# Kernel tuning notes

Hardware: AMD Instinct MI355X
Metric: run time of the kernel (lower is better)

## Reference

```python
import jax, jax.numpy as jnp
import numpy as np

GN_GROUPS = 32
GN_EPS = 1e-5
K = 3  # deform kernel size, padding=1, dilation=1


def conv1x1(x, w):  # x [B,C,H,W], w [O,C]
    return jnp.einsum('bchw,oc->bohw', x, w)


def conv3x3(x, w):  # w [O,I,3,3], stride 1, pad 1
    return jax.lax.conv_general_dilated(
        x, w, window_strides=(1, 1), padding=((1, 1), (1, 1)),
        dimension_numbers=('NCHW', 'OIHW', 'NCHW'))


def group_norm(x, gamma, beta):
    B, C, H, W = x.shape
    xg = x.reshape(B, GN_GROUPS, C // GN_GROUPS, H, W)
    mu = xg.mean(axis=(2, 3, 4), keepdims=True)
    var = xg.var(axis=(2, 3, 4), keepdims=True)
    xn = ((xg - mu) * jax.lax.rsqrt(var + GN_EPS)).reshape(B, C, H, W)
    return xn * gamma[None, :, None, None] + beta[None, :, None, None]


def deform_conv(x, offset, w):
    """DeformConv v1, kernel 3, pad 1, deformable_groups=1.
    x [B,C,H,W]; offset [B,18,H,W] as (dy,dx) per kernel tap; w [O,C,3,3]."""
    B, C, H, W = x.shape
    off = offset.reshape(B, K * K, 2, H, W)
    dy, dx = off[:, :, 0], off[:, :, 1]                      # [B,9,H,W]
    ky, kx = jnp.meshgrid(jnp.arange(K) - 1, jnp.arange(K) - 1, indexing='ij')
    ky = ky.reshape(1, K * K, 1, 1).astype(x.dtype)
    kx = kx.reshape(1, K * K, 1, 1).astype(x.dtype)
    gy = jnp.arange(H, dtype=x.dtype).reshape(1, 1, H, 1)
    gx = jnp.arange(W, dtype=x.dtype).reshape(1, 1, 1, W)
    py = gy + ky + dy                                        # [B,9,H,W] sample y
    px = gx + kx + dx                                        # [B,9,H,W] sample x

    y0 = jnp.floor(py); x0 = jnp.floor(px)
    wy1 = py - y0; wy0 = 1.0 - wy1
    wx1 = px - x0; wx0 = 1.0 - wx1
    xf = x.reshape(B, C, H * W)

    def corner(yc, xc, wgt):
        valid = (yc >= 0) & (yc < H) & (xc >= 0) & (xc < W)  # zero padding outside
        yi = jnp.clip(yc, 0, H - 1).astype(jnp.int32)
        xi = jnp.clip(xc, 0, W - 1).astype(jnp.int32)
        idx = (yi * W + xi).reshape(B, -1)                   # [B, 9*H*W]
        v = jax.vmap(lambda f, i: f[:, i])(xf, idx)          # [B, C, 9*H*W]
        v = v.reshape(B, C, K * K, H, W)
        return v * (wgt * valid.astype(x.dtype))[:, None]

    sampled = (corner(y0, x0, wy0 * wx0) + corner(y0, x0 + 1, wy0 * wx1)
               + corner(y0 + 1, x0, wy1 * wx0) + corner(y0 + 1, x0 + 1, wy1 * wx1))
    # contract sampled [B,C,9,H,W] with weights [O,C,9]
    return jnp.einsum('bckhw,ock->bohw', sampled, w.reshape(w.shape[0], C, K * K))


def setup_inputs() -> dict:
    key = jax.random.key(0)
    ks = jax.random.split(key, 8)
    B, Cc, H, W = 4, 256, 128, 128
    ci = Cc // 4  # 64
    x = jax.random.normal(ks[0], (B, Cc, H, W), dtype=jnp.float32)
    w1 = jax.random.normal(ks[1], (ci, Cc), dtype=jnp.float32) * 0.05
    g1 = jnp.ones((ci,), jnp.float32); b1 = jnp.zeros((ci,), jnp.float32)
    w_off = jax.random.normal(ks[2], (18, ci, 3, 3), dtype=jnp.float32) * 0.01
    w_def = jax.random.normal(ks[3], (ci, ci, 3, 3), dtype=jnp.float32) * 0.05
    w3 = jax.random.normal(ks[4], (Cc, ci), dtype=jnp.float32) * 0.05
    g3 = jnp.ones((Cc,), jnp.float32); b3 = jnp.zeros((Cc,), jnp.float32)
    return {'x': x, 'w1': w1, 'g1': g1, 'b1': b1, 'w_off': w_off,
            'w_def': w_def, 'w3': w3, 'g3': g3, 'b3': b3}


def reference(x, w1, g1, b1, w_off, w_def, w3, g3, b3):
    xd = jax.nn.relu(group_norm(conv1x1(x, w1), g1, b1))     # scale1
    offset1 = conv3x3(xd, w_off)                              # off_conva
    out1 = deform_conv(xd, offset1, w_def)                    # kernel_conva
    out = out1 + xd
    out = jax.nn.relu(group_norm(conv1x1(out, w3), g3, b3)) + x  # scale3 + residual
    return out
```

## Files before the change

kernel.cpp:

```cpp
#include <hip/hip_runtime.h>


#define HW 16384
#define WIDTH 128

typedef __attribute__((ext_vector_type(8))) short bf16x8;
typedef __attribute__((ext_vector_type(4))) float f32x4;

__device__ __forceinline__ unsigned short f2bf(float f) {
  unsigned int u = __float_as_uint(f);
  u = (u + 0x7fffu + ((u >> 16) & 1u)) >> 16;
  return (unsigned short)u;
}
__device__ __forceinline__ float bflo(unsigned int u) { return __uint_as_float(u << 16); }
__device__ __forceinline__ float bfhi(unsigned int u) { return __uint_as_float(u & 0xffff0000u); }

__global__ __launch_bounds__(256) void k_prep(const float* __restrict__ w1, const float* __restrict__ w3,
                                              const float* __restrict__ wdef, const float* __restrict__ woff,
                                              unsigned short* __restrict__ wA1f,
                                              unsigned short* __restrict__ wBf,
                                              unsigned short* __restrict__ wofBf,
                                              unsigned short* __restrict__ w3Bf) {
  int i = blockIdx.x * 256 + threadIdx.x;
  if (i < 16384) {
    int j = i & 7;
    int lane = (i >> 3) & 63;
    int m = (i >> 9) & 3;
    int kt = i >> 11;
    int o = (m << 4) + (lane & 15);
    int c = kt * 32 + ((lane >> 4) << 3) + j;
    wA1f[i] = f2bf(w1[(size_t)o * 256 + c]);
  }
  if (i < 36864) {
    int j = i & 7;
    int lane = (i >> 3) & 63;
    int n = (i >> 9) & 3;
    int kt = i >> 11;
    int kk = kt * 32 + ((lane >> 4) << 3) + j;
    int tap = kk >> 6, c = kk & 63;
    int o = (n << 4) + (lane & 15);
    wBf[i] = f2bf(wdef[(size_t)o * 576 + c * 9 + tap]);
  }
  if (i < 18432) {
    int j = i & 7;
    int lane = (i >> 3) & 63;
    int n = (i >> 9) & 1;
    int kt = i >> 10;
    int kk = kt * 32 + ((lane >> 4) << 3) + j;
    int tap = kk >> 6, c = kk & 63;
    int o = (n << 4) + (lane & 15);
    wofBf[i] = (o < 18) ? f2bf(woff[((size_t)(o * 64 + c)) * 9 + tap]) : (unsigned short)0;
  }
  if (i < 32768) {
    int j = i & 7;
    int lane = (i >> 3) & 63;
    int n = (i >> 9) & 15;
    int kt = i >> 13;
    int c = kt * 32 + ((lane >> 4) << 3) + j;
    int o = (n << 4) + (lane & 15);
    w3Bf[i] = f2bf(w3[(size_t)o * 64 + c]);
  }
}

__global__ __launch_bounds__(256) void k_conv1m(const float* __restrict__ x,
                                                const unsigned short* __restrict__ wA1f,
                                                unsigned short* __restrict__ xdT, float* __restrict__ ps) {
  __shared__ unsigned short xs[2][64][72];
  __shared__ float lds_s[4][32], lds_ss[4][32];
  int tid = threadIdx.x;
  int wave = tid >> 6, lane = tid & 63;
  int b = blockIdx.x >> 8;
  int chunk = blockIdx.x & 255;
  int px0 = chunk << 6;
  int pxl = lane & 15, q = lane >> 4;
  const float* xb = x + (size_t)b * 256 * HW + px0;
  const bf16x8* wAp = (const bf16x8*)wA1f;
  int sc = tid >> 4;
  int sq = tid & 15;
  f32x4 acc[4];
#pragma unroll
  for (int m = 0; m < 4; m++) acc[m] = (f32x4){0.f, 0.f, 0.f, 0.f};

  float4 vr[4];
#pragma unroll
  for (int r = 0; r < 4; r++)
    vr[r] = *(const float4*)(xb + (size_t)(r * 16 + sc) * HW + sq * 4);
#pragma unroll
  for (int r = 0; r < 4; r++) {
    int c = r * 16 + sc;
    xs[0][sq * 4 + 0][c] = f2bf(vr[r].x);
    xs[0][sq * 4 + 1][c] = f2bf(vr[r].y);
    xs[0][sq * 4 + 2][c] = f2bf(vr[r].z);
    xs[0][sq * 4 + 3][c] = f2bf(vr[r].w);
  }
  __syncthreads();

  for (int cb = 0; cb < 4; cb++) {
    int cur = cb & 1;
    if (cb < 3) {
#pragma unroll
      for (int r = 0; r < 4; r++)
        vr[r] = *(const float4*)(xb + (size_t)((cb + 1) * 64 + r * 16 + sc) * HW + sq * 4);
    }
#pragma unroll
    for (int kt = 0; kt < 2; kt++) {
      bf16x8 bfrag = *(const bf16x8*)&xs[cur][wave * 16 + pxl][kt * 32 + q * 8];
      int ktG = cb * 2 + kt;
#pragma unroll
      for (int m = 0; m < 4; m++) {
        bf16x8 af = wAp[(ktG * 4 + m) * 64 + lane];
        acc[m] = __builtin_amdgcn_mfma_f32_16x16x32_bf16(af, bfrag, acc[m], 0, 0, 0);
      }
    }
    if (cb < 3) {
#pragma unroll
      for (int r = 0; r < 4; r++) {
        int c = r * 16 + sc;
        xs[cur ^ 1][sq * 4 + 0][c] = f2bf(vr[r].x);
        xs[cur ^ 1][sq * 4 + 1][c] = f2bf(vr[r].y);
        xs[cur ^ 1][sq * 4 + 2][c] = f2bf(vr[r].z);
        xs[cur ^ 1][sq * 4 + 3][c] = f2bf(vr[r].w);
      }
    }
    __syncthreads();
  }
  unsigned short* xo = xdT + ((size_t)b * HW + px0 + wave * 16 + pxl) * 64 + (q << 2);
#pragma unroll
  for (int m = 0; m < 4; m++) {
    unsigned int u0, u1;
    asm("v_cvt_pk_bf16_f32 %0, %1, %2" : "=v"(u0) : "v"(acc[m][0]), "v"(acc[m][1]));
    asm("v_cvt_pk_bf16_f32 %0, %1, %2" : "=v"(u1) : "v"(acc[m][2]), "v"(acc[m][3]));
    *(uint2*)(xo + m * 16) = make_uint2(u0, u1);
  }
  float s[8], sq2[8];
#pragma unroll
  for (int m = 0; m < 4; m++)
#pragma unroll
    for (int h = 0; h < 2; h++) {
      float a = acc[m][2 * h] + acc[m][2 * h + 1];
      float qq = acc[m][2 * h] * acc[m][2 * h] + acc[m][2 * h + 1] * acc[m][2 * h + 1];
      s[m * 2 + h] = a; sq2[m * 2 + h] = qq;
    }
#pragma unroll
  for (int i = 0; i < 8; i++) {
#pragma unroll
    for (int off = 8; off; off >>= 1) {
      s[i] += __shfl_down(s[i], off, 16);
      sq2[i] += __shfl_down(sq2[i], off, 16);
    }
  }
  if (pxl == 0) {
#pragma unroll
    for (int i = 0; i < 8; i++) {
      int m = i >> 1, h = i & 1;
      int g = m * 8 + q * 2 + h;
      lds_s[wave][g] = s[i];
      lds_ss[wave][g] = sq2[i];
    }
  }
  __syncthreads();
  if (tid < 32) {
    float S = lds_s[0][tid] + lds_s[1][tid] + lds_s[2][tid] + lds_s[3][tid];
    float SS = lds_ss[0][tid] + lds_ss[1][tid] + lds_ss[2][tid] + lds_ss[3][tid];
    int bg = b * 32 + tid;
    ps[(bg * 256 + chunk) * 2] = S;
    ps[(bg * 256 + chunk) * 2 + 1] = SS;
  }
}

__global__ __launch_bounds__(256) void k_gnfin_p(const float* __restrict__ ps, float* __restrict__ mrs,
                                                 int S, float n) {
  int bg = blockIdx.x;
  float s = 0.f, ss = 0.f;
  for (int i = threadIdx.x; i < S; i += 256) { s += ps[(bg * S + i) * 2]; ss += ps[(bg * S + i) * 2 + 1]; }
#pragma unroll
  for (int off = 32; off; off >>= 1) { s += __shfl_down(s, off); ss += __shfl_down(ss, off); }
  __shared__ float ls[4], lss[4];
  int wv = threadIdx.x >> 6;
  if ((threadIdx.x & 63) == 0) { ls[wv] = s; lss[wv] = ss; }
  __syncthreads();
  if (threadIdx.x == 0) {
    float Sa = ls[0] + ls[1] + ls[2] + ls[3];
    float SSa = lss[0] + lss[1] + lss[2] + lss[3];
    float mu = Sa / n;
    float var = SSa / n - mu * mu;
    mrs[bg] = mu;
    mrs[128 + bg] = rsqrtf(var + 1e-5f);
  }
}

__global__ __launch_bounds__(256) void k_gnapply_bf(unsigned short* __restrict__ xdT,
                                                    const float* __restrict__ mrs,
                                                    const float* __restrict__ g1, const float* __restrict__ b1) {
  int i = blockIdx.x * 256 + threadIdx.x;
  int b = i >> 17;
  int ck = i & 7;
  int c0 = ck << 3;
  uint4 v = ((const uint4*)xdT)[i];
  float ga[8], be[8];
#pragma unroll
  for (int j = 0; j < 8; j += 2) {
    int g = (c0 + j) >> 1;
    float mu = mrs[b * 32 + g], rs = mrs[128 + b * 32 + g];
    ga[j] = g1[c0 + j] * rs;     be[j] = b1[c0 + j] - mu * ga[j];
    ga[j + 1] = g1[c0 + j + 1] * rs; be[j + 1] = b1[c0 + j + 1] - mu * ga[j + 1];
  }
  float r[8];
  r[0] = fmaxf(bflo(v.x) * ga[0] + be[0], 0.f);
  r[1] = fmaxf(bfhi(v.x) * ga[1] + be[1], 0.f);
  r[2] = fmaxf(bflo(v.y) * ga[2] + be[2], 0.f);
  r[3] = fmaxf(bfhi(v.y) * ga[3] + be[3], 0.f);
  r[4] = fmaxf(bflo(v.z) * ga[4] + be[4], 0.f);
  r[5] = fmaxf(bfhi(v.z) * ga[5] + be[5], 0.f);
  r[6] = fmaxf(bflo(v.w) * ga[6] + be[6], 0.f);
  r[7] = fmaxf(bfhi(v.w) * ga[7] + be[7], 0.f);
  uint4 o;
  asm("v_cvt_pk_bf16_f32 %0, %1, %2" : "=v"(o.x) : "v"(r[0]), "v"(r[1]));
  asm("v_cvt_pk_bf16_f32 %0, %1, %2" : "=v"(o.y) : "v"(r[2]), "v"(r[3]));
  asm("v_cvt_pk_bf16_f32 %0, %1, %2" : "=v"(o.z) : "v"(r[4]), "v"(r[5]));
  asm("v_cvt_pk_bf16_f32 %0, %1, %2" : "=v"(o.w) : "v"(r[6]), "v"(r[7]));
  ((uint4*)xdT)[i] = o;
}

__global__ __launch_bounds__(576, 7) void k_mega(const unsigned short* __restrict__ xdT,
                                                 const unsigned short* __restrict__ wofBf,
                                                 const unsigned short* __restrict__ wBf,
                                                 const unsigned short* __restrict__ w3Bf,
                                                 unsigned short* __restrict__ t3,
                                                 float* __restrict__ ps2) {
  __shared__ unsigned short A[36 * 65 * 8];
  __shared__ float offsL[64 * 18];
  int tid = threadIdx.x;
  int bb = blockIdx.x >> 8;
  int tileid = blockIdx.x & 255;
  int px0 = tileid << 6;
  const unsigned short* xtf = xdT + (size_t)bb * 64 * HW;
  const char* xbt = (const char*)xtf;
  int wave = tid >> 6;
  int lane = tid & 63;
  int q16 = lane >> 2;
  int ch4 = lane & 3;
  int kcbyte = (wave * 4 + ch4) * 1040;
  int kq = lane >> 4;

  f32x4 aoff = {0.f, 0.f, 0.f, 0.f};
  {
    int ky = wave / 3 - 1, kx = wave % 3 - 1;
    int n2 = wave & 1;
    int mh1 = wave >> 1;
    int r1 = mh1 * 16 + (lane & 15);
    for (int h = 0; h < 2; ++h) {
      int co = (h << 6) + (ch4 << 4);
#pragma unroll
      for (int g = 0; g < 4; ++g) {
        int src = (g << 4) + q16;
        int px = px0 + src;
        int sy = (px >> 7) + ky;
        int sx = (px & 127) + kx;
        bool valid = ((unsigned)sy < 128u) && ((unsigned)sx < 128u);
        uint4 v = make_uint4(0u, 0u, 0u, 0u);
        if (valid) v = *(const uint4*)(xbt + (((sy << 7) + sx) << 7) + co);
        *(uint4*)((char*)A + kcbyte + src * 16) = v;
      }
      __syncthreads();
      if (wave < 8) {
        const bf16x8* wp = (const bf16x8*)wofBf;
        __builtin_amdgcn_s_setprio(1);
#pragma unroll
        for (int tap = 0; tap < 9; ++tap) {
          bf16x8 bk = wp[((2 * tap + h) * 2 + n2) * 64 + lane];
          bf16x8 a0 = *(const bf16x8*)((const char*)A + ((tap * 4 + kq) * 65 + r1) * 16);
          aoff = __builtin_amdgcn_mfma_f32_16x16x32_bf16(a0, bk, aoff, 0, 0, 0);
        }
        __builtin_amdgcn_s_setprio(0);
      }
      __syncthreads();
    }
    if (wave < 8) {
      int o = n2 * 16 + (lane & 15);
      if (o < 18) {
        int prow = mh1 * 16 + ((lane >> 4) << 2);
#pragma unroll
        for (int r = 0; r < 4; r++) offsL[(prow + r) * 18 + o] = aoff[r];
      }
    }
  }
  __syncthreads();

  float w00, w01, w10, w11;
  int a00, a01, a10, a11;
  {
    int px = px0 + lane;
    int y = px >> 7, xc = px & 127;
    float dy = offsL[lane * 18 + 2 * wave];
    float dx = offsL[lane * 18 + 2 * wave + 1];
    float py = (float)(y + wave / 3 - 1) + dy;
    float pxx = (float)(xc + wave % 3 - 1) + dx;
    float y0f = floorf(py), x0f = floorf(pxx);
    float ay = py - y0f, ax = pxx - x0f;
    int y0 = (int)y0f, x0 = (int)x0f;
    int y1i = y0 + 1, x1i = x0 + 1;
    float by0 = 1.f - ay, bx0 = 1.f - ax;
    bool vy0 = (unsigned)y0 < 128u, vy1 = (unsigned)y1i < 128u;
    bool vx0 = (unsigned)x0 < 128u, vx1 = (unsigned)x1i < 128u;
    w00 = (vy0 && vx0) ? by0 * bx0 : 0.f;
    w01 = (vy0 && vx1) ? by0 * ax : 0.f;
    w10 = (vy1 && vx0) ? ay * bx0 : 0.f;
    w11 = (vy1 && vx1) ? ay * ax : 0.f;
    int iy0 = min(max(y0, 0), 127), iy1 = min(max(y1i, 0), 127);
    int ix0 = min(max(x0, 0), 127), ix1 = min(max(x1i, 0), 127);
    a00 = (iy0 * WIDTH + ix0) << 7;
    a01 = (iy0 * WIDTH + ix1) << 7;
    a10 = (iy1 * WIDTH + ix0) << 7;
    a11 = (iy1 * WIDTH + ix1) << 7;
  }

  int n1 = wave & 3;
  int mh = wave >> 2;
  f32x4 acc0 = {0.f, 0.f, 0.f, 0.f};
  f32x4 acc1 = {0.f, 0.f, 0.f, 0.f};
  for (int h = 0; h < 2; ++h) {
    int co = (h << 6) + (ch4 << 4);
#pragma unroll
    for (int g = 0; g < 4; ++g) {
      int src = (g << 4) + q16;
      float j0 = __shfl(w00, src), j1 = __shfl(w01, src);
      float j2 = __shfl(w10, src), j3 = __shfl(w11, src);
      int b0 = __shfl(a00, src), b1 = __shfl(a01, src);
      int b2 = __shfl(a10, src), b3 = __shfl(a11, src);
      uint4 v0 = *(const uint4*)(xbt + b0 + co);
      uint4 v1 = *(const uint4*)(xbt + b1 + co);
      uint4 v2 = *(const uint4*)(xbt + b2 + co);
      uint4 v3 = *(const uint4*)(xbt + b3 + co);
      float r[8];
      r[0] = j0 * bflo(v0.x) + j1 * bflo(v1.x) + j2 * bflo(v2.x) + j3 * bflo(v3.x);
      r[1] = j0 * bfhi(v0.x) + j1 * bfhi(v1.x) + j2 * bfhi(v2.x) + j3 * bfhi(v3.x);
      r[2] = j0 * bflo(v0.y) + j1 * bflo(v1.y) + j2 * bflo(v2.y) + j3 * bflo(v3.y);
      r[3] = j0 * bfhi(v0.y) + j1 * bfhi(v1.y) + j2 * bfhi(v2.y) + j3 * bfhi(v3.y);
      r[4] = j0 * bflo(v0.z) + j1 * bflo(v1.z) + j2 * bflo(v2.z) + j3 * bflo(v3.z);
      r[5] = j0 * bfhi(v0.z) + j1 * bfhi(v1.z) + j2 * bfhi(v2.z) + j3 * bfhi(v3.z);
      r[6] = j0 * bflo(v0.w) + j1 * bflo(v1.w) + j2 * bflo(v2.w) + j3 * bflo(v3.w);
      r[7] = j0 * bfhi(v0.w) + j1 * bfhi(v1.w) + j2 * bfhi(v2.w) + j3 * bfhi(v3.w);
      uint4 ov;
      asm("v_cvt_pk_bf16_f32 %0, %1, %2" : "=v"(ov.x) : "v"(r[0]), "v"(r[1]));
      asm("v_cvt_pk_bf16_f32 %0, %1, %2" : "=v"(ov.y) : "v"(r[2]), "v"(r[3]));
      asm("v_cvt_pk_bf16_f32 %0, %1, %2" : "=v"(ov.z) : "v"(r[4]), "v"(r[5]));
      asm("v_cvt_pk_bf16_f32 %0, %1, %2" : "=v"(ov.w) : "v"(r[6]), "v"(r[7]));
      *(uint4*)((char*)A + kcbyte + src * 16) = ov;
    }
    __syncthreads();
    if (wave < 8) {
      int r0r = mh * 32 + (lane & 15);
      const bf16x8* wp = (const bf16x8*)wBf;
      __builtin_amdgcn_s_setprio(1);
#pragma unroll
      for (int tap = 0; tap < 9; ++tap) {
        bf16x8 bk = wp[((2 * tap + h) * 4 + n1) * 64 + lane];
        int kc = tap * 4 + kq;
        bf16x8 a0 = *(const bf16x8*)((const char*)A + (kc * 65 + r0r) * 16);
        bf16x8 a1 = *(const bf16x8*)((const char*)A + (kc * 65 + r0r + 16) * 16);
        acc0 = __builtin_amdgcn_mfma_f32_16x16x32_bf16(a0, bk, acc0, 0, 0, 0);
        acc1 = __builtin_amdgcn_mfma_f32_16x16x32_bf16(a1, bk, acc1, 0, 0, 0);
      }
      __builtin_amdgcn_s_setprio(0);
    }
    __syncthreads();
  }
  if (wave < 8) {
    int c = n1 * 16 + (lane & 15);
    int pb = px0 + mh * 32 + ((lane >> 4) << 2);
#pragma unroll
    for (int r = 0; r < 4; r++) {
      acc0[r] += __uint_as_float((unsigned int)xtf[(size_t)(pb + r) * 64 + c] << 16);
      acc1[r] += __uint_as_float((unsigned int)xtf[(size_t)(pb + 16 + r) * 64 + c] << 16);
    }
    char* base = (char*)A + (c >> 3) * 1040 + (c & 7) * 2;
    int pxr = mh * 32 + ((lane >> 4) << 2);
#pragma unroll
    for (int r = 0; r < 4; r++) {
      *(unsigned short*)(base + (size_t)(pxr + r) * 16) = f2bf(acc0[r]);
      *(unsigned short*)(base + (size_t)(pxr + 16 + r) * 16) = f2bf(acc1[r]);
    }
  }
  __syncthreads();
  if (wave >= 8) return;

  f32x4 cA[4], cB[4];
#pragma unroll
  for (int ni = 0; ni < 4; ni++) {
    cA[ni] = (f32x4){0.f, 0.f, 0.f, 0.f};
    cB[ni] = (f32x4){0.f, 0.f, 0.f, 0.f};
  }
  {
    int mt0 = (wave >> 2) * 2;
    const bf16x8* wp2 = (const bf16x8*)w3Bf;
    __builtin_amdgcn_s_setprio(1);
#pragma unroll
    for (int kt = 0; kt < 2; kt++) {
      int kc = kt * 4 + kq;
      bf16x8 aA = *(const bf16x8*)((const char*)A + (size_t)(kc * 65 + mt0 * 16 + (lane & 15)) * 16);
      bf16x8 aB = *(const bf16x8*)((const char*)A + (size_t)(kc * 65 + (mt0 + 1) * 16 + (lane & 15)) * 16);
#pragma unroll
      for (int ni = 0; ni < 4; ni++) {
        int ng = n1 * 4 + ni;
        bf16x8 bk = wp2[(kt * 16 + ng) * 64 + lane];
        cA[ni] = __builtin_amdgcn_mfma_f32_16x16x32_bf16(aA, bk, cA[ni], 0, 0, 0);
        cB[ni] = __builtin_amdgcn_mfma_f32_16x16x32_bf16(aB, bk, cB[ni], 0, 0, 0);
      }
    }
    __builtin_amdgcn_s_setprio(0);
  }
#pragma unroll
  for (int ni = 0; ni < 4; ni++) {
    float s = 0.f, qq = 0.f;
#pragma unroll
    for (int r = 0; r < 4; r++) {
      float v0 = cA[ni][r], v1 = cB[ni][r];
      s += v0 + v1; qq += v0 * v0 + v1 * v1;
    }
    s += __shfl_down(s, 32); qq += __shfl_down(qq, 32);
    s += __shfl_down(s, 16); qq += __shfl_down(qq, 16);
    s += __shfl_down(s, 4);  qq += __shfl_down(qq, 4);
    s += __shfl_down(s, 2);  qq += __shfl_down(qq, 2);
    s += __shfl_down(s, 1);  qq += __shfl_down(qq, 1);
    if (lane == 0 || lane == 8) {
      int g = (n1 * 4 + ni) * 2 + (lane >> 3);
      int slot = ((bb * 32 + g) * 256 + tileid) * 2 + (wave >> 2);
      ps2[slot * 2] = s;
      ps2[slot * 2 + 1] = qq;
    }
  }
  unsigned short* tb = t3 + (size_t)bb * 256 * HW + px0;
  int mtq = (wave >> 2) * 32 + ((lane >> 4) << 2);
#pragma unroll
  for (int ni = 0; ni < 4; ni++) {
    int o = (n1 * 4 + ni) * 16 + (lane & 15);
    unsigned short* p0 = tb + (size_t)o * HW + mtq;
    unsigned int u0, u1, u2, u3;
    asm("v_cvt_pk_bf16_f32 %0, %1, %2" : "=v"(u0) : "v"(cA[ni][0]), "v"(cA[ni][1]));
    asm("v_cvt_pk_bf16_f32 %0, %1, %2" : "=v"(u1) : "v"(cA[ni][2]), "v"(cA[ni][3]));
    asm("v_cvt_pk_bf16_f32 %0, %1, %2" : "=v"(u2) : "v"(cB[ni][0]), "v"(cB[ni][1]));
    asm("v_cvt_pk_bf16_f32 %0, %1, %2" : "=v"(u3) : "v"(cB[ni][2]), "v"(cB[ni][3]));
    *(uint2*)p0 = make_uint2(u0, u1);
    *(uint2*)(p0 + 16) = make_uint2(u2, u3);
  }
}

__global__ __launch_bounds__(256) void k_final(const unsigned short* __restrict__ t3, const float* __restrict__ x,
                                               const float* __restrict__ mrs, const float* __restrict__ g3,
                                               const float* __restrict__ b3, float* __restrict__ out) {
  int i4 = blockIdx.x * 256 + threadIdx.x;
  int b = i4 >> 20;
  int c = (i4 >> 12) & 255;
  int g = c >> 3;
  float mu = mrs[b * 32 + g], rs = mrs[128 + b * 32 + g];
  float ga = g3[c] * rs, be = b3[c] - mu * ga;
  uint2 tv = ((const uint2*)t3)[i4];
  float t0 = bflo(tv.x);
  float t1 = bfhi(tv.x);
  float t2 = bflo(tv.y);
  float t3v = bfhi(tv.y);
  float4 xv = ((const float4*)x)[i4];
  float4 r;
  r.x = fmaxf(t0 * ga + be, 0.f) + xv.x;
  r.y = fmaxf(t1 * ga + be, 0.f) + xv.y;
  r.z = fmaxf(t2 * ga + be, 0.f) + xv.z;
  r.w = fmaxf(t3v * ga + be, 0.f) + xv.w;
  ((float4*)out)[i4] = r;
}

extern "C" void kernel_launch(void* const* d_in, const int* in_sizes, int n_in,
                              void* d_out, int out_size, void* d_ws, size_t ws_size,
                              hipStream_t stream) {
  const float* x    = (const float*)d_in[0];
  const float* w1   = (const float*)d_in[1];
  const float* g1   = (const float*)d_in[2];
  const float* b1   = (const float*)d_in[3];
  const float* woff = (const float*)d_in[4];
  const float* wdef = (const float*)d_in[5];
  const float* w3   = (const float*)d_in[6];
  const float* g3   = (const float*)d_in[7];
  const float* b3   = (const float*)d_in[8];
  float* ws = (float*)d_ws;

  unsigned short* xdT = (unsigned short*)ws;
  unsigned short* t3  = (unsigned short*)(ws + 2097152);
  float* base = ws + 2097152 + 8388608;
  float* mrs1 = base;
  float* mrs2 = mrs1 + 256;
  unsigned short* wA1f  = (unsigned short*)(mrs2 + 256);
  unsigned short* wBf   = (unsigned short*)(mrs2 + 256 + 8192);
  unsigned short* wofBf = (unsigned short*)(mrs2 + 256 + 8192 + 18432);
  unsigned short* w3Bf  = (unsigned short*)(mrs2 + 256 + 8192 + 18432 + 9216);
  float* ps   = mrs2 + 256 + 8192 + 18432 + 9216 + 16384;
  float* ps2  = ps + 65536;
  float* out  = (float*)d_out;

  hipLaunchKernelGGL(k_prep, dim3(144), dim3(256), 0, stream, w1, w3, wdef, woff, wA1f, wBf, wofBf, w3Bf);
  hipLaunchKernelGGL(k_conv1m, dim3(1024), dim3(256), 0, stream, x, wA1f, xdT, ps);
  hipLaunchKernelGGL(k_gnfin_p, dim3(128), dim3(256), 0, stream, ps, mrs1, 256, (float)(2 * HW));
  hipLaunchKernelGGL(k_gnapply_bf, dim3(2048), dim3(256), 0, stream, xdT, mrs1, g1, b1);
  hipLaunchKernelGGL(k_mega, dim3(1024), dim3(576), 0, stream, xdT, wofBf, wBf, w3Bf, t3, ps2);
  hipLaunchKernelGGL(k_gnfin_p, dim3(128), dim3(256), 0, stream, ps2, mrs2, 512, 131072.f);
  hipLaunchKernelGGL(k_final, dim3(16384), dim3(256), 0, stream, t3, x, mrs2, g3, b3, out);
}
```

Before: 111.1 us.

## Build deform-conv MFMA A operands in registers instead of staging through LDS

The bilinear sampling step is restructured so each wave computes sample coordinates and weights per tap for its own pixel row and packs the interpolated bf16 values directly into the MFMA A-fragment. This removes the shuffle-based distribution, the LDS write of the sampled matrix, and the two __syncthreads per half, and only waves 0-7 take part. The cost is that the waves sharing a row block each recompute the same sampling and gathers, and all 16 waves no longer share the gather work. Register pressure may also rise.

```diff
diff --git a/kernel.cpp b/kernel.cpp
--- a/kernel.cpp
+++ b/kernel.cpp
@@ -287,104 +287,91 @@
   }
   __syncthreads();
 
-  float w00, w01, w10, w11;
-  int a00, a01, a10, a11;
-  {
-    int px = px0 + lane;
-    int y = px >> 7, xc = px & 127;
-    float dy = offsL[lane * 18 + 2 * wave];
-    float dx = offsL[lane * 18 + 2 * wave + 1];
-    float py = (float)(y + wave / 3 - 1) + dy;
-    float pxx = (float)(xc + wave % 3 - 1) + dx;
-    float y0f = floorf(py), x0f = floorf(pxx);
-    float ay = py - y0f, ax = pxx - x0f;
-    int y0 = (int)y0f, x0 = (int)x0f;
-    int y1i = y0 + 1, x1i = x0 + 1;
-    float by0 = 1.f - ay, bx0 = 1.f - ax;
-    bool vy0 = (unsigned)y0 < 128u, vy1 = (unsigned)y1i < 128u;
-    bool vx0 = (unsigned)x0 < 128u, vx1 = (unsigned)x1i < 128u;
-    w00 = (vy0 && vx0) ? by0 * bx0 : 0.f;
-    w01 = (vy0 && vx1) ? by0 * ax : 0.f;
-    w10 = (vy1 && vx0) ? ay * bx0 : 0.f;
-    w11 = (vy1 && vx1) ? ay * ax : 0.f;
-    int iy0 = min(max(y0, 0), 127), iy1 = min(max(y1i, 0), 127);
-    int ix0 = min(max(x0, 0), 127), ix1 = min(max(x1i, 0), 127);
-    a00 = (iy0 * WIDTH + ix0) << 7;
-    a01 = (iy0 * WIDTH + ix1) << 7;
-    a10 = (iy1 * WIDTH + ix0) << 7;
-    a11 = (iy1 * WIDTH + ix1) << 7;
-  }
-
-  int n1 = wave & 3;
-  int mh = wave >> 2;
-  f32x4 acc0 = {0.f, 0.f, 0.f, 0.f};
-  f32x4 acc1 = {0.f, 0.f, 0.f, 0.f};
-  for (int h = 0; h < 2; ++h) {
-    int co = (h << 6) + (ch4 << 4);
-#pragma unroll
-    for (int g = 0; g < 4; ++g) {
-      int src = (g << 4) + q16;
-      float j0 = __shfl(w00, src), j1 = __shfl(w01, src);
-      float j2 = __shfl(w10, src), j3 = __shfl(w11, src);
-      int b0 = __shfl(a00, src), b1 = __shfl(a01, src);
-      int b2 = __shfl(a10, src), b3 = __shfl(a11, src);
-      uint4 v0 = *(const uint4*)(xbt + b0 + co);
-      uint4 v1 = *(const uint4*)(xbt + b1 + co);
-      uint4 v2 = *(const uint4*)(xbt + b2 + co);
-      uint4 v3 = *(const uint4*)(xbt + b3 + co);
-      float r[8];
-      r[0] = j0 * bflo(v0.x) + j1 * bflo(v1.x) + j2 * bflo(v2.x) + j3 * bflo(v3.x);
-      r[1] = j0 * bfhi(v0.x) + j1 * bfhi(v1.x) + j2 * bfhi(v2.x) + j3 * bfhi(v3.x);
-      r[2] = j0 * bflo(v0.y) + j1 * bflo(v1.y) + j2 * bflo(v2.y) + j3 * bflo(v3.y);
-      r[3] = j0 * bfhi(v0.y) + j1 * bfhi(v1.y) + j2 * bfhi(v2.y) + j3 * bfhi(v3.y);
-      r[4] = j0 * bflo(v0.z) + j1 * bflo(v1.z) + j2 * bflo(v2.z) + j3 * bflo(v3.z);
-      r[5] = j0 * bfhi(v0.z) + j1 * bfhi(v1.z) + j2 * bfhi(v2.z) + j3 * bfhi(v3.z);
-      r[6] = j0 * bflo(v0.w) + j1 * bflo(v1.w) + j2 * bflo(v2.w) + j3 * bflo(v3.w);
-      r[7] = j0 * bfhi(v0.w) + j1 * bfhi(v1.w) + j2 * bfhi(v2.w) + j3 * bfhi(v3.w);
-      uint4 ov;
-      asm("v_cvt_pk_bf16_f32 %0, %1, %2" : "=v"(ov.x) : "v"(r[0]), "v"(r[1]));
-      asm("v_cvt_pk_bf16_f32 %0, %1, %2" : "=v"(ov.y) : "v"(r[2]), "v"(r[3]));
-      asm("v_cvt_pk_bf16_f32 %0, %1, %2" : "=v"(ov.z) : "v"(r[4]), "v"(r[5]));
-      asm("v_cvt_pk_bf16_f32 %0, %1, %2" : "=v"(ov.w) : "v"(r[6]), "v"(r[7]));
-      *(uint4*)((char*)A + kcbyte + src * 16) = ov;
-    }
-    __syncthreads();
-    if (wave < 8) {
-      int r0r = mh * 32 + (lane & 15);
-      const bf16x8* wp = (const bf16x8*)wBf;
-      __builtin_amdgcn_s_setprio(1);
-#pragma unroll
-      for (int tap = 0; tap < 9; ++tap) {
-        bf16x8 bk = wp[((2 * tap + h) * 4 + n1) * 64 + lane];
-        int kc = tap * 4 + kq;
-        bf16x8 a0 = *(const bf16x8*)((const char*)A + (kc * 65 + r0r) * 16);
-        bf16x8 a1 = *(const bf16x8*)((const char*)A + (kc * 65 + r0r + 16) * 16);
-        acc0 = __builtin_amdgcn_mfma_f32_16x16x32_bf16(a0, bk, acc0, 0, 0, 0);
-        acc1 = __builtin_amdgcn_mfma_f32_16x16x32_bf16(a1, bk, acc1, 0, 0, 0);
-      }
-      __builtin_amdgcn_s_setprio(0);
-    }
-    __syncthreads();
-  }
+  f32x4 accA = {0.f, 0.f, 0.f, 0.f};
+  f32x4 accB = {0.f, 0.f, 0.f, 0.f};
+  int pxl = lane & 15;
+  int dmh = wave >> 1, dnh = wave & 1;
   if (wave < 8) {
-    int c = n1 * 16 + (lane & 15);
-    int pb = px0 + mh * 32 + ((lane >> 4) << 2);
+    int rowl = dmh * 16 + pxl;
+    int pxg = px0 + rowl;
+    int yy = pxg >> 7, xx = pxg & 127;
+    const bf16x8* wp = (const bf16x8*)wBf;
+#pragma unroll 2
+    for (int tap = 0; tap < 9; ++tap) {
+      float dy = offsL[rowl * 18 + 2 * tap];
+      float dx = offsL[rowl * 18 + 2 * tap + 1];
+      float py = (float)(yy + tap / 3 - 1) + dy;
+      float pxx = (float)(xx + tap % 3 - 1) + dx;
+      float y0f = floorf(py), x0f = floorf(pxx);
+      float ay = py - y0f, ax = pxx - x0f;
+      int y0 = (int)y0f, x0 = (int)x0f;
+      int y1i = y0 + 1, x1i = x0 + 1;
+      float by0 = 1.f - ay, bx0 = 1.f - ax;
+      bool vy0 = (unsigned)y0 < 128u, vy1 = (unsigned)y1i < 128u;
+      bool vx0 = (unsigned)x0 < 128u, vx1 = (unsigned)x1i < 128u;
+      float w00 = (vy0 && vx0) ? by0 * bx0 : 0.f;
+      float w01 = (vy0 && vx1) ? by0 * ax : 0.f;
+      float w10 = (vy1 && vx0) ? ay * bx0 : 0.f;
+      float w11 = (vy1 && vx1) ? ay * ax : 0.f;
+      int iy0 = min(max(y0, 0), 127), iy1 = min(max(y1i, 0), 127);
+      int ix0 = min(max(x0, 0), 127), ix1 = min(max(x1i, 0), 127);
+      int a00 = (iy0 * WIDTH + ix0) << 7;
+      int a01 = (iy0 * WIDTH + ix1) << 7;
+      int a10 = (iy1 * WIDTH + ix0) << 7;
+      int a11 = (iy1 * WIDTH + ix1) << 7;
+#pragma unroll
+      for (int h = 0; h < 2; ++h) {
+        int co = (h << 6) + (kq << 4);
+        uint4 v0 = *(const uint4*)(xbt + a00 + co);
+        uint4 v1 = *(const uint4*)(xbt + a01 + co);
+        uint4 v2 = *(const uint4*)(xbt + a10 + co);
+        uint4 v3 = *(const uint4*)(xbt + a11 + co);
+        float r[8];
+        r[0] = w00 * bflo(v0.x) + w01 * bflo(v1.x) + w10 * bflo(v2.x) + w11 * bflo(v3.x);
+        r[1] = w00 * bfhi(v0.x) + w01 * bfhi(v1.x) + w10 * bfhi(v2.x) + w11 * bfhi(v3.x);
+        r[2] = w00 * bflo(v0.y) + w01 * bflo(v1.y) + w10 * bflo(v2.y) + w11 * bflo(v3.y);
+        r[3] = w00 * bfhi(v0.y) + w01 * bfhi(v1.y) + w10 * bfhi(v2.y) + w11 * bfhi(v3.y);
+        r[4] = w00 * bflo(v0.z) + w01 * bflo(v1.z) + w10 * bflo(v2.z) + w11 * bflo(v3.z);
+        r[5] = w00 * bfhi(v0.z) + w01 * bfhi(v1.z) + w10 * bfhi(v2.z) + w11 * bfhi(v3.z);
+        r[6] = w00 * bflo(v0.w) + w01 * bflo(v1.w) + w10 * bflo(v2.w) + w11 * bflo(v3.w);
+        r[7] = w00 * bfhi(v0.w) + w01 * bfhi(v1.w) + w10 * bfhi(v2.w) + w11 * bfhi(v3.w);
+        bf16x8 af;
+        unsigned int u0, u1, u2, u3;
+        asm("v_cvt_pk_bf16_f32 %0, %1, %2" : "=v"(u0) : "v"(r[0]), "v"(r[1]));
+        asm("v_cvt_pk_bf16_f32 %0, %1, %2" : "=v"(u1) : "v"(r[2]), "v"(r[3]));
+        asm("v_cvt_pk_bf16_f32 %0, %1, %2" : "=v"(u2) : "v"(r[4]), "v"(r[5]));
+        asm("v_cvt_pk_bf16_f32 %0, %1, %2" : "=v"(u3) : "v"(r[6]), "v"(r[7]));
+        ((unsigned int*)&af)[0] = u0;
+        ((unsigned int*)&af)[1] = u1;
+        ((unsigned int*)&af)[2] = u2;
+        ((unsigned int*)&af)[3] = u3;
+        int kt = tap * 2 + h;
+        bf16x8 bk0 = wp[(kt * 4 + dnh * 2 + 0) * 64 + lane];
+        bf16x8 bk1 = wp[(kt * 4 + dnh * 2 + 1) * 64 + lane];
+        accA = __builtin_amdgcn_mfma_f32_16x16x32_bf16(af, bk0, accA, 0, 0, 0);
+        accB = __builtin_amdgcn_mfma_f32_16x16x32_bf16(af, bk1, accB, 0, 0, 0);
+      }
+    }
+    int c0 = dnh * 32 + pxl;
+    int pb = px0 + dmh * 16 + (kq << 2);
 #pragma unroll
     for (int r = 0; r < 4; r++) {
-      acc0[r] += __uint_as_float((unsigned int)xtf[(size_t)(pb + r) * 64 + c] << 16);
-      acc1[r] += __uint_as_float((unsigned int)xtf[(size_t)(pb + 16 + r) * 64 + c] << 16);
-    }
-    char* base = (char*)A + (c >> 3) * 1040 + (c & 7) * 2;
-    int pxr = mh * 32 + ((lane >> 4) << 2);
+      accA[r] += __uint_as_float((unsigned int)xtf[(size_t)(pb + r) * 64 + c0] << 16);
+      accB[r] += __uint_as_float((unsigned int)xtf[(size_t)(pb + r) * 64 + c0 + 16] << 16);
+    }
+    int pxr = dmh * 16 + (kq << 2);
+    char* bA = (char*)A + (c0 >> 3) * 1040 + (c0 & 7) * 2;
+    char* bB = (char*)A + ((c0 + 16) >> 3) * 1040 + ((c0 + 16) & 7) * 2;
 #pragma unroll
     for (int r = 0; r < 4; r++) {
-      *(unsigned short*)(base + (size_t)(pxr + r) * 16) = f2bf(acc0[r]);
-      *(unsigned short*)(base + (size_t)(pxr + 16 + r) * 16) = f2bf(acc1[r]);
+      *(unsigned short*)(bA + (size_t)(pxr + r) * 16) = f2bf(accA[r]);
+      *(unsigned short*)(bB + (size_t)(pxr + r) * 16) = f2bf(accB[r]);
     }
   }
   __syncthreads();
   if (wave >= 8) return;
 
+  int n1 = wave & 3;
   f32x4 cA[4], cB[4];
 #pragma unroll
   for (int ni = 0; ni < 4; ni++) {
```

Measured after the change: 154.0 us. +38.7%, slower.

## Drop ninth wave in deform mega kernel and alias offset buffer onto LDS tile

Applied to the files above, without the earlier changes.

Block size for the fused deform kernel goes from 576 to 512 threads. The ninth tap's gather and bilinear-sample work, previously done by its own wave, is spread across waves 0-3 as extra per-lane work. The separate shared offset buffer is removed and aliased onto the A tile, with an added barrier before A is overwritten. The aim is to cut LDS and wave overhead so more blocks fit per CU, at the cost of uneven load on waves 0-3 and one extra sync.

```diff
diff --git a/kernel.cpp b/kernel.cpp
--- a/kernel.cpp
+++ b/kernel.cpp
@@ -222,14 +222,14 @@
   ((uint4*)xdT)[i] = o;
 }
 
-__global__ __launch_bounds__(576, 7) void k_mega(const unsigned short* __restrict__ xdT,
+__global__ __launch_bounds__(512, 8) void k_mega(const unsigned short* __restrict__ xdT,
                                                  const unsigned short* __restrict__ wofBf,
                                                  const unsigned short* __restrict__ wBf,
                                                  const unsigned short* __restrict__ w3Bf,
                                                  unsigned short* __restrict__ t3,
                                                  float* __restrict__ ps2) {
   __shared__ unsigned short A[36 * 65 * 8];
-  __shared__ float offsL[64 * 18];
+  float* offsL = (float*)A;
   int tid = threadIdx.x;
   int bb = blockIdx.x >> 8;
   int tileid = blockIdx.x & 255;
@@ -240,12 +240,13 @@
   int lane = tid & 63;
   int q16 = lane >> 2;
   int ch4 = lane & 3;
-  int kcbyte = (wave * 4 + ch4) * 1040;
   int kq = lane >> 4;
 
   f32x4 aoff = {0.f, 0.f, 0.f, 0.f};
   {
-    int ky = wave / 3 - 1, kx = wave % 3 - 1;
+    int kyA = wave / 3 - 1, kxA = wave % 3 - 1;
+    int kcbA = (wave * 4 + ch4) * 1040;
+    int kcb8 = (32 + ch4) * 1040;
     int n2 = wave & 1;
     int mh1 = wave >> 1;
     int r1 = mh1 * 16 + (lane & 15);
@@ -255,15 +256,25 @@
       for (int g = 0; g < 4; ++g) {
         int src = (g << 4) + q16;
         int px = px0 + src;
-        int sy = (px >> 7) + ky;
-        int sx = (px & 127) + kx;
+        int sy = (px >> 7) + kyA;
+        int sx = (px & 127) + kxA;
         bool valid = ((unsigned)sy < 128u) && ((unsigned)sx < 128u);
         uint4 v = make_uint4(0u, 0u, 0u, 0u);
         if (valid) v = *(const uint4*)(xbt + (((sy << 7) + sx) << 7) + co);
-        *(uint4*)((char*)A + kcbyte + src * 16) = v;
+        *(uint4*)((char*)A + kcbA + src * 16) = v;
+      }
+      if (wave < 4) {
+        int src = (wave << 4) + q16;
+        int px = px0 + src;
+        int sy = (px >> 7) + 1;
+        int sx = (px & 127) + 1;
+        bool valid = ((unsigned)sy < 128u) && ((unsigned)sx < 128u);
+        uint4 v = make_uint4(0u, 0u, 0u, 0u);
+        if (valid) v = *(const uint4*)(xbt + (((sy << 7) + sx) << 7) + co);
+        *(uint4*)((char*)A + kcb8 + src * 16) = v;
       }
       __syncthreads();
-      if (wave < 8) {
+      {
         const bf16x8* wp = (const bf16x8*)wofBf;
         __builtin_amdgcn_s_setprio(1);
 #pragma unroll
@@ -276,7 +287,7 @@
       }
       __syncthreads();
     }
-    if (wave < 8) {
+    {
       int o = n2 * 16 + (lane & 15);
       if (o < 18) {
         int prow = mh1 * 16 + ((lane >> 4) << 2);
@@ -314,11 +325,41 @@
     a10 = (iy1 * WIDTH + ix0) << 7;
     a11 = (iy1 * WIDTH + ix1) << 7;
   }
+  float e00 = 0.f, e01 = 0.f, e10 = 0.f, e11 = 0.f;
+  int b00 = 0, b01 = 0, b10 = 0, b11 = 0;
+  if (wave < 4) {
+    int px = px0 + lane;
+    int y = px >> 7, xc = px & 127;
+    float dy = offsL[lane * 18 + 16];
+    float dx = offsL[lane * 18 + 17];
+    float py = (float)(y + 1) + dy;
+    float pxx = (float)(xc + 1) + dx;
+    float y0f = floorf(py), x0f = floorf(pxx);
+    float ay = py - y0f, ax = pxx - x0f;
+    int y0 = (int)y0f, x0 = (int)x0f;
+    int y1i = y0 + 1, x1i = x0 + 1;
+    float by0 = 1.f - ay, bx0 = 1.f - ax;
+    bool vy0 = (unsigned)y0 < 128u, vy1 = (unsigned)y1i < 128u;
+    bool vx0 = (unsigned)x0 < 128u, vx1 = (unsigned)x1i < 128u;
+    e00 = (vy0 && vx0) ? by0 * bx0 : 0.f;
+    e01 = (vy0 && vx1) ? by0 * ax : 0.f;
+    e10 = (vy1 && vx0) ? ay * bx0 : 0.f;
+    e11 = (vy1 && vx1) ? ay * ax : 0.f;
+    int iy0 = min(max(y0, 0), 127), iy1 = min(max(y1i, 0), 127);
+    int ix0 = min(max(x0, 0), 127), ix1 = min(max(x1i, 0), 127);
+    b00 = (iy0 * WIDTH + ix0) << 7;
+    b01 = (iy0 * WIDTH + ix1) << 7;
+    b10 = (iy1 * WIDTH + ix0) << 7;
+    b11 = (iy1 * WIDTH + ix1) << 7;
+  }
+  __syncthreads();
 
   int n1 = wave & 3;
   int mh = wave >> 2;
   f32x4 acc0 = {0.f, 0.f, 0.f, 0.f};
   f32x4 acc1 = {0.f, 0.f, 0.f, 0.f};
+  int kcbA = (wave * 4 + ch4) * 1040;
+  int kcb8 = (32 + ch4) * 1040;
   for (int h = 0; h < 2; ++h) {
     int co = (h << 6) + (ch4 << 4);
 #pragma unroll
@@ -326,12 +367,12 @@
       int src = (g << 4) + q16;
       float j0 = __shfl(w00, src), j1 = __shfl(w01, src);
       float j2 = __shfl(w10, src), j3 = __shfl(w11, src);
-      int b0 = __shfl(a00, src), b1 = __shfl(a01, src);
-      int b2 = __shfl(a10, src), b3 = __shfl(a11, src);
-      uint4 v0 = *(const uint4*)(xbt + b0 + co);
-      uint4 v1 = *(const uint4*)(xbt + b1 + co);
-      uint4 v2 = *(const uint4*)(xbt + b2 + co);
-      uint4 v3 = *(const uint4*)(xbt + b3 + co);
+      int c0 = __shfl(a00, src), c1 = __shfl(a01, src);
+      int c2 = __shfl(a10, src), c3 = __shfl(a11, src);
+      uint4 v0 = *(const uint4*)(xbt + c0 + co);
+      uint4 v1 = *(const uint4*)(xbt + c1 + co);
+      uint4 v2 = *(const uint4*)(xbt + c2 + co);
+      uint4 v3 = *(const uint4*)(xbt + c3 + co);
       float r[8];
       r[0] = j0 * bflo(v0.x) + j1 * bflo(v1.x) + j2 * bflo(v2.x) + j3 * bflo(v3.x);
       r[1] = j0 * bfhi(v0.x) + j1 * bfhi(v1.x) + j2 * bfhi(v2.x) + j3 * bfhi(v3.x);
@@ -346,10 +387,36 @@
       asm("v_cvt_pk_bf16_f32 %0, %1, %2" : "=v"(ov.y) : "v"(r[2]), "v"(r[3]));
       asm("v_cvt_pk_bf16_f32 %0, %1, %2" : "=v"(ov.z) : "v"(r[4]), "v"(r[5]));
       asm("v_cvt_pk_bf16_f32 %0, %1, %2" : "=v"(ov.w) : "v"(r[6]), "v"(r[7]));
-      *(uint4*)((char*)A + kcbyte + src * 16) = ov;
+      *(uint4*)((char*)A + kcbA + src * 16) = ov;
+    }
+    if (wave < 4) {
+      int src = (wave << 4) + q16;
+      float j0 = __shfl(e00, src), j1 = __shfl(e01, src);
+      float j2 = __shfl(e10, src), j3 = __shfl(e11, src);
+      int c0 = __shfl(b00, src), c1 = __shfl(b01, src);
+      int c2 = __shfl(b10, src), c3 = __shfl(b11, src);
+      uint4 v0 = *(const uint4*)(xbt + c0 + co);
+      uint4 v1 = *(const uint4*)(xbt + c1 + co);
+      uint4 v2 = *(const uint4*)(xbt + c2 + co);
+      uint4 v3 = *(const uint4*)(xbt + c3 + co);
+      float r[8];
+      r[0] = j0 * bflo(v0.x) + j1 * bflo(v1.x) + j2 * bflo(v2.x) + j3 * bflo(v3.x);
+      r[1] = j0 * bfhi(v0.x) + j1 * bfhi(v1.x) + j2 * bfhi(v2.x) + j3 * bfhi(v3.x);
+      r[2] = j0 * bflo(v0.y) + j1 * bflo(v1.y) + j2 * bflo(v2.y) + j3 * bflo(v3.y);
+      r[3] = j0 * bfhi(v0.y) + j1 * bfhi(v1.y) + j2 * bfhi(v2.y) + j3 * bfhi(v3.y);
+      r[4] = j0 * bflo(v0.z) + j1 * bflo(v1.z) + j2 * bflo(v2.z) + j3 * bflo(v3.z);
+      r[5] = j0 * bfhi(v0.z) + j1 * bfhi(v1.z) + j2 * bfhi(v2.z) + j3 * bfhi(v3.z);
+      r[6] = j0 * bflo(v0.w) + j1 * bflo(v1.w) + j2 * bflo(v2.w) + j3 * bflo(v3.w);
+      r[7] = j0 * bfhi(v0.w) + j1 * bfhi(v1.w) + j2 * bfhi(v2.w) + j3 * bfhi(v3.w);
+      uint4 ov;
+      asm("v_cvt_pk_bf16_f32 %0, %1, %2" : "=v"(ov.x) : "v"(r[0]), "v"(r[1]));
+      asm("v_cvt_pk_bf16_f32 %0, %1, %2" : "=v"(ov.y) : "v"(r[2]), "v"(r[3]));
+      asm("v_cvt_pk_bf16_f32 %0, %1, %2" : "=v"(ov.z) : "v"(r[4]), "v"(r[5]));
+      asm("v_cvt_pk_bf16_f32 %0, %1, %2" : "=v"(ov.w) : "v"(r[6]), "v"(r[7]));
+      *(uint4*)((char*)A + kcb8 + src * 16) = ov;
     }
     __syncthreads();
-    if (wave < 8) {
+    {
       int r0r = mh * 32 + (lane & 15);
       const bf16x8* wp = (const bf16x8*)wBf;
       __builtin_amdgcn_s_setprio(1);
@@ -366,7 +433,7 @@
     }
     __syncthreads();
   }
-  if (wave < 8) {
+  {
     int c = n1 * 16 + (lane & 15);
     int pb = px0 + mh * 32 + ((lane >> 4) << 2);
 #pragma unroll
@@ -383,7 +450,6 @@
     }
   }
   __syncthreads();
-  if (wave >= 8) return;
 
   f32x4 cA[4], cB[4];
 #pragma unroll
@@ -500,7 +566,7 @@
   hipLaunchKernelGGL(k_conv1m, dim3(1024), dim3(256), 0, stream, x, wA1f, xdT, ps);
   hipLaunchKernelGGL(k_gnfin_p, dim3(128), dim3(256), 0, stream, ps, mrs1, 256, (float)(2 * HW));
   hipLaunchKernelGGL(k_gnapply_bf, dim3(2048), dim3(256), 0, stream, xdT, mrs1, g1, b1);
-  hipLaunchKernelGGL(k_mega, dim3(1024), dim3(576), 0, stream, xdT, wofBf, wBf, w3Bf, t3, ps2);
+  hipLaunchKernelGGL(k_mega, dim3(1024), dim3(512), 0, stream, xdT, wofBf, wBf, w3Bf, t3, ps2);
   hipLaunchKernelGGL(k_gnfin_p, dim3(128), dim3(256), 0, stream, ps2, mrs2, 512, 131072.f);
   hipLaunchKernelGGL(k_final, dim3(16384), dim3(256), 0, stream, t3, x, mrs2, g3, b3, out);
 }
```

New measurement: 112.3 us. No clear change (+1.1%).
